# Kernel optimization log

Hardware: AMD Instinct MI355X
Metric: run time of the kernel (lower is better)

## Reference

```python
import jax, jax.numpy as jnp
import numpy as np
from jax import lax

H_LSTM = 2048

def setup_inputs() -> dict:
    key = jax.random.key(0)
    ks = jax.random.split(key, 8)
    N, T = 32, 20
    inp = {
        'base_out': jax.random.normal(ks[0], (N * T, 12, 4096), jnp.float32) * 0.1,
        'dist': jax.random.uniform(ks[1], (N, T, 2, 2, 12, 12), jnp.float32),
        'W1': jax.random.normal(ks[2], (4096, 4096), jnp.float32) * 0.02,
        'W2': jax.random.normal(ks[3], (2048, 2048), jnp.float32) * 0.02,
        'w_ih': jax.random.normal(ks[4], (4 * H_LSTM, 3072), jnp.float32) * 0.02,
        'w_hh': jax.random.normal(ks[5], (4 * H_LSTM, H_LSTM), jnp.float32) * 0.02,
        'b_ih': jnp.zeros((4 * H_LSTM,), jnp.float32),
        'b_hh': jnp.zeros((4 * H_LSTM,), jnp.float32),
        'Wc': jax.random.normal(ks[6], (8, H_LSTM), jnp.float32) * 0.01,
        'bc': jnp.zeros((8,), jnp.float32),
        'N': N,
        'T': T,
    }
    return inp

def _lstm(x, w_ih, w_hh, b_ih, b_hh):
    # x: [seq, batch, in]; torch gate order i, f, g, o
    seq, batch, _ = x.shape
    h0 = jnp.zeros((batch, H_LSTM), x.dtype)
    def step(carry, xt):
        h, c = carry
        gates = xt @ w_ih.T + b_ih + h @ w_hh.T + b_hh
        i, f, g, o = jnp.split(gates, 4, axis=-1)
        c = jax.nn.sigmoid(f) * c + jax.nn.sigmoid(i) * jnp.tanh(g)
        h = jax.nn.sigmoid(o) * jnp.tanh(c)
        return (h, c), h
    (_, _), hs = lax.scan(step, (h0, h0), x)
    return hs  # [seq, batch, H]

def reference(base_out, dist, W1, W2, w_ih, w_hh, b_ih, b_hh, Wc, bc, N, T):
    NT = N * T
    distb = dist[:, :, 1].reshape(NT, 2, 12, 12)
    distc = dist[:, :, 0].reshape(NT, 2, 12, 12)
    # conv1da: 1x1 conv == per-node linear; base_out [NT,12,4096] -> [NT,4096,12]
    node1 = jnp.einsum('oc,nvc->nov', W1, base_out).reshape(NT, 2, 2048, 12)
    n1 = jnp.einsum('nkcv,nkvw->ncw', node1, distb) + jnp.einsum('nkcv,nkvw->ncw', node1, distc)
    node1 = jax.nn.relu(n1)  # [NT,2048,12]
    node2 = jnp.einsum('oc,ncv->nov', W2, node1).reshape(NT, 2, 1024, 12)
    n2b = jax.nn.relu(jnp.einsum('nkcv,nkvw->ncw', node2, distb))  # [NT,1024,12]
    n2c = jax.nn.relu(jnp.einsum('nkcv,nkvw->ncw', node2, distc))
    left = n2b[:, :, :6].mean(axis=2)
    right = n2b[:, :, 6:].mean(axis=2)
    allf = n2c.mean(axis=2)
    pooled = jnp.concatenate([left, right, allf], axis=1).reshape(N, T, 3072)
    # torch nn.LSTM default is seq-first: sequence dim = N, batch dim = T (faithful)
    video_feat = _lstm(pooled, w_ih, w_hh, b_ih, b_hh)  # [N, T, 2048]
    group_cls = video_feat[:, -1, :] @ Wc.T + bc  # [N, num_classes]
    return group_cls, video_feat
```

## Files before the change

kernel.cpp:

```cpp
#include <hip/hip_runtime.h>

typedef _Float16 f16x8 __attribute__((ext_vector_type(8)));
typedef _Float16 f16x4 __attribute__((ext_vector_type(4)));
typedef __attribute__((ext_vector_type(4))) float f32x4;
typedef __attribute__((ext_vector_type(4))) unsigned int u32x4;

#define DI __device__ __forceinline__

DI void gload16(const void* g, void* l) {
  __builtin_amdgcn_global_load_lds(
      (const __attribute__((address_space(1))) unsigned int*)g,
      (__attribute__((address_space(3))) unsigned int*)l, 16, 0, 0);
}

DI float sigm(float x) { return 1.f / (1.f + __expf(-x)); }
DI float tanh_(float x) { return 2.f / (1.f + __expf(-2.f * x)) - 1.f; }

__global__ __launch_bounds__(256) void cvt4h(const float* __restrict__ in,
                                             _Float16* __restrict__ out, int n4) {
  int i = blockIdx.x * 256 + threadIdx.x;
  if (i >= n4) return;
  float4 v = ((const float4*)in)[i];
  f16x4 o;
  o[0] = (_Float16)v.x; o[1] = (_Float16)v.y; o[2] = (_Float16)v.z; o[3] = (_Float16)v.w;
  ((f16x4*)out)[i] = o;
}

__global__ __launch_bounds__(512, 2)
void gemm256(const _Float16* __restrict__ A, const _Float16* __restrict__ B,
             _Float16* __restrict__ C, int M, int N, int K) {
  extern __shared__ _Float16 sm[];
  _Float16* smA = sm;
  _Float16* smB = sm + 32768;

  const int t512 = threadIdx.x;
  const int lane = t512 & 63, wid = t512 >> 6;
  const int wm = (wid >> 2) * 128, wn = (wid & 3) * 64;
  const int lr = lane & 15, lg = lane >> 4;
  const int sg0 = lg ^ (lr & 7), sg1 = (4 + lg) ^ (lr & 7);

  const int nwgx = gridDim.x;
  int id = blockIdx.y * nwgx + blockIdx.x;
  int nwg = nwgx * gridDim.y;
  if ((nwg & 7) == 0) id = (id & 7) * (nwg >> 3) + (id >> 3);
  const int n0 = (id % nwgx) * 256;
  const int m0 = (id / nwgx) * 256;

  f32x4 acc[8][4] = {};

#define STAGE(kt, buf)                                                         \
  {                                                                            \
    const int kbase = (kt) * 64;                                               \
    _Pragma("unroll") for (int i = 0; i < 4; ++i) {                            \
      int G = t512 + i * 512;                                                  \
      int r = G >> 3, gs = (G & 7) ^ (r & 7);                                  \
      gload16(A + (size_t)(m0 + r) * K + kbase + gs * 8,                       \
              smA + (buf) * 16384 + G * 8);                                    \
    }                                                                          \
    _Pragma("unroll") for (int i = 0; i < 4; ++i) {                            \
      int G = t512 + i * 512;                                                  \
      int r = G >> 3, gs = (G & 7) ^ (r & 7);                                  \
      gload16(B + (size_t)(n0 + r) * K + kbase + gs * 8,                       \
              smB + (buf) * 16384 + G * 8);                                    \
    }                                                                          \
  }

#define KPHASE(SG)                                                             \
  {                                                                            \
    f16x8 av[8], bv[4];                                                        \
    _Pragma("unroll") for (int im = 0; im < 8; ++im)                           \
      av[im] = *(const f16x8*)(Ab + (wm + im * 16 + lr) * 128 + (SG) * 16);    \
    _Pragma("unroll") for (int jn = 0; jn < 4; ++jn)                           \
      bv[jn] = *(const f16x8*)(Bb + (wn + jn * 16 + lr) * 128 + (SG) * 16);    \
    __builtin_amdgcn_s_barrier();                                              \
    asm volatile("s_waitcnt lgkmcnt(0)" ::: "memory");                         \
    __builtin_amdgcn_sched_barrier(0);                                         \
    __builtin_amdgcn_s_setprio(1);                                             \
    _Pragma("unroll") for (int im = 0; im < 8; ++im)                           \
        _Pragma("unroll") for (int jn = 0; jn < 4; ++jn)                       \
      acc[im][jn] = __builtin_amdgcn_mfma_f32_16x16x32_f16(av[im], bv[jn],     \
                                                           acc[im][jn], 0, 0, 0); \
    __builtin_amdgcn_s_setprio(0);                                             \
    __builtin_amdgcn_s_barrier();                                              \
    __builtin_amdgcn_sched_barrier(0);                                         \
  }

  STAGE(0, 0);
  const int NT = K >> 6;
  for (int t = 0; t < NT; ++t) {
    const int c = t & 1;
    if (t + 1 < NT) {
      STAGE(t + 1, c ^ 1);
      asm volatile("s_waitcnt vmcnt(8)" ::: "memory");
    } else {
      asm volatile("s_waitcnt vmcnt(0)" ::: "memory");
    }
    __builtin_amdgcn_s_barrier();
    __builtin_amdgcn_sched_barrier(0);
    const char* Ab = (const char*)(smA + c * 16384);
    const char* Bb = (const char*)(smB + c * 16384);
    KPHASE(sg0)
    KPHASE(sg1)
  }
#undef STAGE
#undef KPHASE

#pragma unroll
  for (int m = 0; m < 8; ++m)
#pragma unroll
    for (int n = 0; n < 4; ++n)
#pragma unroll
      for (int q = 0; q < 4; ++q) {
        int row = m0 + wm + m * 16 + lg * 4 + q;
        int col = n0 + wn + n * 16 + lr;
        C[(size_t)row * N + col] = (_Float16)acc[m][n][q];
      }
}

template <int OUTMODE>
__global__ __launch_bounds__(256, 2)
void gemm_bt(const _Float16* __restrict__ A, const _Float16* __restrict__ B,
             void* __restrict__ Cout, const float* __restrict__ bias1,
             const float* __restrict__ bias2, int M, int N, int K) {
  __shared__ alignas(16) _Float16 Asm[128 * 32];
  __shared__ alignas(16) _Float16 Bsm[128 * 32];
  const int t = threadIdx.x;
  const int lane = t & 63, wid = t >> 6;
  const int m0 = blockIdx.y * 128, n0 = blockIdx.x * 128;
  const int wm = (wid >> 1) * 64, wn = (wid & 1) * 64;
  const int lr = lane & 15, lk = (lane >> 4) * 8, lg = lane >> 4;

  f32x4 acc[4][4] = {};

  const int e0 = t, e1 = t + 256;
  const int ra0 = e0 >> 2, ka0 = (e0 & 3) << 3;
  const int ra1 = e1 >> 2, ka1 = (e1 & 3) << 3;

  for (int kt = 0; kt < K; kt += 32) {
    gload16(A + (size_t)(m0 + ra0) * K + kt + ka0, &Asm[e0 * 8]);
    gload16(A + (size_t)(m0 + ra1) * K + kt + ka1, &Asm[e1 * 8]);
    gload16(B + (size_t)(n0 + ra0) * K + kt + ka0, &Bsm[e0 * 8]);
    gload16(B + (size_t)(n0 + ra1) * K + kt + ka1, &Bsm[e1 * 8]);
    __syncthreads();
    f16x8 af[4], bfr[4];
#pragma unroll
    for (int f = 0; f < 4; ++f) {
      af[f] = *(const f16x8*)&Asm[(wm + f * 16 + lr) * 32 + lk];
      bfr[f] = *(const f16x8*)&Bsm[(wn + f * 16 + lr) * 32 + lk];
    }
#pragma unroll
    for (int i = 0; i < 4; ++i)
#pragma unroll
      for (int j = 0; j < 4; ++j)
        acc[i][j] = __builtin_amdgcn_mfma_f32_16x16x32_f16(af[i], bfr[j], acc[i][j], 0, 0, 0);
    __syncthreads();
  }

#pragma unroll
  for (int i = 0; i < 4; ++i) {
#pragma unroll
    for (int j = 0; j < 4; ++j) {
#pragma unroll
      for (int q = 0; q < 4; ++q) {
        int row = m0 + wm + i * 16 + lg * 4 + q;
        int col = n0 + wn + j * 16 + lr;
        if constexpr (OUTMODE == 0) {
          ((_Float16*)Cout)[(size_t)row * N + col] = (_Float16)acc[i][j][q];
        } else {
          ((float*)Cout)[(size_t)row * N + col] = acc[i][j][q] + bias1[col] + bias2[col];
        }
      }
    }
  }
}

__global__ __launch_bounds__(256) void mix1(const _Float16* __restrict__ node1,
                                            const float* __restrict__ dist,
                                            _Float16* __restrict__ n1t) {
  __shared__ float ds[288];
  const int nt = blockIdx.x, tid = threadIdx.x;
  for (int i = tid; i < 288; i += 256)
    ds[i] = dist[(size_t)nt * 576 + 288 + i] + dist[(size_t)nt * 576 + i];
  __syncthreads();
  const int c = blockIdx.y * 256 + tid;
  float s[12];
#pragma unroll
  for (int w = 0; w < 12; ++w) s[w] = 0.f;
#pragma unroll
  for (int k = 0; k < 2; ++k)
#pragma unroll
    for (int v = 0; v < 12; ++v) {
      float x = (float)node1[(size_t)(nt * 12 + v) * 4096 + k * 2048 + c];
      const float* d = &ds[k * 144 + v * 12];
#pragma unroll
      for (int w = 0; w < 12; ++w) s[w] = fmaf(x, d[w], s[w]);
    }
#pragma unroll
  for (int w = 0; w < 12; ++w)
    n1t[(size_t)(nt * 12 + w) * 2048 + c] = (_Float16)fmaxf(s[w], 0.f);
}

__global__ __launch_bounds__(256) void mix2(const _Float16* __restrict__ node2,
                                            const float* __restrict__ dist,
                                            _Float16* __restrict__ pooled) {
  __shared__ float db[288], dc[288];
  const int nt = blockIdx.x, tid = threadIdx.x;
  for (int i = tid; i < 288; i += 256) {
    db[i] = dist[(size_t)nt * 576 + 288 + i];
    dc[i] = dist[(size_t)nt * 576 + i];
  }
  __syncthreads();
  const int c = blockIdx.y * 256 + tid;
  float sb[12], sc[12];
#pragma unroll
  for (int w = 0; w < 12; ++w) { sb[w] = 0.f; sc[w] = 0.f; }
#pragma unroll
  for (int k = 0; k < 2; ++k)
#pragma unroll
    for (int v = 0; v < 12; ++v) {
      float x = (float)node2[(size_t)(nt * 12 + v) * 2048 + k * 1024 + c];
      const float* pb = &db[k * 144 + v * 12];
      const float* pc = &dc[k * 144 + v * 12];
#pragma unroll
      for (int w = 0; w < 12; ++w) { sb[w] = fmaf(x, pb[w], sb[w]); sc[w] = fmaf(x, pc[w], sc[w]); }
    }
  float left = 0.f, right = 0.f, allf = 0.f;
#pragma unroll
  for (int w = 0; w < 6; ++w) left += fmaxf(sb[w], 0.f);
#pragma unroll
  for (int w = 6; w < 12; ++w) right += fmaxf(sb[w], 0.f);
#pragma unroll
  for (int w = 0; w < 12; ++w) allf += fmaxf(sc[w], 0.f);
  pooled[(size_t)nt * 3072 + c] = (_Float16)(left * (1.f / 6.f));
  pooled[(size_t)nt * 3072 + 1024 + c] = (_Float16)(right * (1.f / 6.f));
  pooled[(size_t)nt * 3072 + 2048 + c] = (_Float16)(allf * (1.f / 12.f));
}

__global__ __launch_bounds__(256, 1) void lstm_persist3(
    const _Float16* __restrict__ whh,
    const float* __restrict__ xg,
    _Float16* __restrict__ hbuf,
    float* __restrict__ vf,
    int* __restrict__ go,
    int* __restrict__ flags) {
  extern __shared__ char lds[];
  char* hls = lds;
  char* wls = lds + 81920;
  float* Y = (float*)(lds + 147456);
  const int tid = threadIdx.x, bid = blockIdx.x, cb = bid * 8;
  const int lane = tid & 63, wid = tid >> 6;
  const int mi = wid >> 1, ni = wid & 1;
  const int lr = lane & 15, lg = lane >> 4;
  const int n = ni * 16 + lr;
  const _Float16* wp = whh + (size_t)((n >> 3) * 2048 + cb + (n & 7)) * 2048;
  const int arow = mi * 16 + lr;
  const int arow_c = (arow < 20) ? arow : (16 + (lr & 3));
  const int axor = arow_c & 7;
  const int pt = tid >> 3, pj = tid & 7;
  float c_reg = 0.f;

  for (int i = tid; i < 4096; i += 256) {
    int r = i >> 8, gg = i & 255;
    u32x4 v = *(const u32x4*)(whh + (size_t)((r >> 3) * 2048 + cb + (r & 7)) * 2048 + gg * 8);
    *(u32x4*)(wls + (((r) << 8) + (gg ^ (r & 7))) * 16) = v;
  }

  for (int s = 0; s < 32; ++s) {
    if (s > 0) {
      const _Float16* hsrc = hbuf + ((s - 1) & 1) * 65536;
      u32x4 tmp[20];
#pragma unroll
      for (int j = 0; j < 20; ++j) {
        asm volatile("global_load_dwordx4 %0, %1, off sc0 sc1"
                     : "=v"(tmp[j]) : "v"(hsrc + j * 2048 + tid * 8));
      }
      asm volatile("s_waitcnt vmcnt(0)" ::: "memory");
      __builtin_amdgcn_sched_barrier(0);
#pragma unroll
      for (int j = 0; j < 20; ++j)
        *(u32x4*)(hls + (((j) << 8) + (tid ^ (j & 7))) * 16) = tmp[j];
      __syncthreads();
      f32x4 acc = {};
      if (ni == 0) {
#pragma unroll 8
        for (int kt = 0; kt < 2048; kt += 32) {
          int g = (kt >> 3) + lg;
          f16x8 a = *(const f16x8*)(hls + ((arow_c << 8) + (g ^ axor)) * 16);
          f16x8 w = *(const f16x8*)(wls + ((n << 8) + (g ^ (n & 7))) * 16);
          acc = __builtin_amdgcn_mfma_f32_16x16x32_f16(a, w, acc, 0, 0, 0);
        }
      } else {
#pragma unroll 8
        for (int kt = 0; kt < 2048; kt += 32) {
          int g = (kt >> 3) + lg;
          f16x8 a = *(const f16x8*)(hls + ((arow_c << 8) + (g ^ axor)) * 16);
          f16x8 w = *(const f16x8*)(wp + kt + lg * 8);
          acc = __builtin_amdgcn_mfma_f32_16x16x32_f16(a, w, acc, 0, 0, 0);
        }
      }
#pragma unroll
      for (int q = 0; q < 4; ++q) {
        int t = mi * 16 + lg * 4 + q;
        if (t < 20) Y[t * 32 + n] = acc[q];
      }
    }
    __syncthreads();
    if (tid < 160) {
      float g0 = xg[(size_t)(s * 20 + pt) * 8192 + cb + pj];
      float g1 = xg[(size_t)(s * 20 + pt) * 8192 + 2048 + cb + pj];
      float g2 = xg[(size_t)(s * 20 + pt) * 8192 + 4096 + cb + pj];
      float g3 = xg[(size_t)(s * 20 + pt) * 8192 + 6144 + cb + pj];
      if (s > 0) {
        g0 += Y[pt * 32 + pj];
        g1 += Y[pt * 32 + 8 + pj];
        g2 += Y[pt * 32 + 16 + pj];
        g3 += Y[pt * 32 + 24 + pj];
      }
      float cn = sigm(g1) * c_reg + sigm(g0) * tanh_(g2);
      float hv = sigm(g3) * tanh_(cn);
      c_reg = cn;
      union { _Float16 f; unsigned short u; } cv;
      cv.f = (_Float16)hv;
      int mine = cv.u;
      int oth = __shfl_xor(mine, 1, 64);
      if ((tid & 1) == 0) {
        unsigned int packed = ((unsigned)mine & 0xffffu) | ((unsigned)oth << 16);
        __hip_atomic_store((unsigned int*)(hbuf + (s & 1) * 65536 + pt * 2048 + cb + pj),
                           packed, __ATOMIC_RELAXED, __HIP_MEMORY_SCOPE_AGENT);
      }
      vf[(size_t)(s * 20 + pt) * 2048 + cb + pj] = hv;
    }
    if (s == 31) break;
    asm volatile("s_waitcnt vmcnt(0)" ::: "memory");
    __syncthreads();
    if (bid == 0) {
      if (tid > 0) {
        while (__hip_atomic_load(&flags[tid * 16], __ATOMIC_RELAXED,
                                 __HIP_MEMORY_SCOPE_AGENT) < s + 1)
          __builtin_amdgcn_s_sleep(2);
      }
      __syncthreads();
      if (tid < 8)
        __hip_atomic_store(&go[tid * 16], s + 1, __ATOMIC_RELAXED,
                           __HIP_MEMORY_SCOPE_AGENT);
    } else {
      if (tid == 0) {
        __hip_atomic_store(&flags[bid * 16], s + 1, __ATOMIC_RELAXED,
                           __HIP_MEMORY_SCOPE_AGENT);
        while (__hip_atomic_load(&go[(bid & 7) * 16], __ATOMIC_RELAXED,
                                 __HIP_MEMORY_SCOPE_AGENT) < s + 1)
          __builtin_amdgcn_s_sleep(4);
      }
      __syncthreads();
    }
  }
}

__global__ __launch_bounds__(256) void gcls(const float* __restrict__ vf,
                                            const float* __restrict__ Wc,
                                            const float* __restrict__ bc,
                                            float* __restrict__ out) {
  const int n = blockIdx.x;
  const int j = threadIdx.x >> 5, l = threadIdx.x & 31;
  const float* v = vf + (size_t)(n * 20 + 19) * 2048;
  const float* w = Wc + (size_t)j * 2048;
  float s = 0.f;
  for (int c = l; c < 2048; c += 32) s += v[c] * w[c];
  for (int off = 16; off > 0; off >>= 1) s += __shfl_down(s, off, 32);
  if (l == 0) out[n * 8 + j] = s + bc[j];
}

extern "C" void kernel_launch(void* const* d_in, const int* in_sizes, int n_in,
                              void* d_out, int out_size, void* d_ws, size_t ws_size,
                              hipStream_t stream) {
  const float* base_out = (const float*)d_in[0];
  const float* dist = (const float*)d_in[1];
  const float* W1 = (const float*)d_in[2];
  const float* W2 = (const float*)d_in[3];
  const float* w_ih = (const float*)d_in[4];
  const float* w_hh = (const float*)d_in[5];
  const float* b_ih = (const float*)d_in[6];
  const float* b_hh = (const float*)d_in[7];
  const float* Wc = (const float*)d_in[8];
  const float* bc = (const float*)d_in[9];
  float* out = (float*)d_out;

  char* ws = (char*)d_ws;
  const size_t MB = 1048576;
  _Float16* Ahf   = (_Float16*)(ws + 0);
  _Float16* W1hf  = (_Float16*)(ws + 60 * MB);
  _Float16* node1 = (_Float16*)(ws + 92 * MB);
  _Float16* whhhf = (_Float16*)(ws + 152 * MB);
  _Float16* wihhf = (_Float16*)(ws + 184 * MB);
  float* xg       = (float*)(ws + 232 * MB);
  int* go         = (int*)(ws + 252 * MB);
  int* flags      = (int*)(ws + 252 * MB + 1024);
  _Float16* hbuf  = (_Float16*)(ws + 252 * MB + 65536);
  _Float16* W2hf  = (_Float16*)(ws + 255 * MB);
  _Float16* pooled= (_Float16*)(ws + 263 * MB);
  _Float16* n1t   = (_Float16*)(ws + 0);
  _Float16* node2 = (_Float16*)(ws + 30 * MB);

  hipFuncSetAttribute((const void*)gemm256,
                      hipFuncAttributeMaxDynamicSharedMemorySize, 131072);
  hipFuncSetAttribute((const void*)lstm_persist3,
                      hipFuncAttributeMaxDynamicSharedMemorySize, 150016);

  cvt4h<<<30720, 256, 0, stream>>>(base_out, Ahf, 7864320);
  cvt4h<<<16384, 256, 0, stream>>>(W1, W1hf, 4194304);
  cvt4h<<<4096, 256, 0, stream>>>(W2, W2hf, 1048576);
  cvt4h<<<24576, 256, 0, stream>>>(w_ih, wihhf, 6291456);
  cvt4h<<<16384, 256, 0, stream>>>(w_hh, whhhf, 4194304);

  gemm256<<<dim3(16, 30), 512, 131072, stream>>>(Ahf, W1hf, node1, 7680, 4096, 4096);
  mix1<<<dim3(640, 8), 256, 0, stream>>>(node1, dist, n1t);
  gemm256<<<dim3(8, 30), 512, 131072, stream>>>(n1t, W2hf, node2, 7680, 2048, 2048);
  mix2<<<dim3(640, 4), 256, 0, stream>>>(node2, dist, pooled);
  gemm_bt<1><<<dim3(64, 5), 256, 0, stream>>>(pooled, wihhf, xg, b_ih, b_hh,
                                              640, 8192, 3072);
  hipMemsetAsync(go, 0, 65536, stream);
  lstm_persist3<<<256, 256, 150016, stream>>>(whhhf, xg, hbuf, out + 256, go, flags);
  gcls<<<32, 256, 0, stream>>>(out + 256, Wc, bc, out);
}
```

Before: 834.8 us.

## Restructure GEMM main loop into four sub-tile phases with interleaved prefetch

Reorganizes the 256x256 fp16 GEMM inner loop into four quadrant phases (8 MFMAs per k-slice pair each). LDS fragment loads for the next quadrant and global-to-LDS prefetch of the next K tile (A then B) are spread across the phases. This cuts register use for fragments and aims to overlap memory traffic with MFMA work. It adds more barriers per iteration and requires a full vmcnt(0) wait at the end of every iteration.

```diff
diff --git a/kernel.cpp b/kernel.cpp
--- a/kernel.cpp
+++ b/kernel.cpp
@@ -48,7 +48,7 @@
 
   f32x4 acc[8][4] = {};
 
-#define STAGE(kt, buf)                                                         \
+#define STAGE_A(kt, buf)                                                       \
   {                                                                            \
     const int kbase = (kt) * 64;                                               \
     _Pragma("unroll") for (int i = 0; i < 4; ++i) {                            \
@@ -57,6 +57,10 @@
       gload16(A + (size_t)(m0 + r) * K + kbase + gs * 8,                       \
               smA + (buf) * 16384 + G * 8);                                    \
     }                                                                          \
+  }
+#define STAGE_B(kt, buf)                                                       \
+  {                                                                            \
+    const int kbase = (kt) * 64;                                               \
     _Pragma("unroll") for (int i = 0; i < 4; ++i) {                            \
       int G = t512 + i * 512;                                                  \
       int r = G >> 3, gs = (G & 7) ^ (r & 7);                                  \
@@ -65,45 +69,87 @@
     }                                                                          \
   }
 
-#define KPHASE(SG)                                                             \
-  {                                                                            \
-    f16x8 av[8], bv[4];                                                        \
-    _Pragma("unroll") for (int im = 0; im < 8; ++im)                           \
-      av[im] = *(const f16x8*)(Ab + (wm + im * 16 + lr) * 128 + (SG) * 16);    \
-    _Pragma("unroll") for (int jn = 0; jn < 4; ++jn)                           \
-      bv[jn] = *(const f16x8*)(Bb + (wn + jn * 16 + lr) * 128 + (SG) * 16);    \
-    __builtin_amdgcn_s_barrier();                                              \
-    asm volatile("s_waitcnt lgkmcnt(0)" ::: "memory");                         \
-    __builtin_amdgcn_sched_barrier(0);                                         \
-    __builtin_amdgcn_s_setprio(1);                                             \
-    _Pragma("unroll") for (int im = 0; im < 8; ++im)                           \
-        _Pragma("unroll") for (int jn = 0; jn < 4; ++jn)                       \
-      acc[im][jn] = __builtin_amdgcn_mfma_f32_16x16x32_f16(av[im], bv[jn],     \
-                                                           acc[im][jn], 0, 0, 0); \
-    __builtin_amdgcn_s_setprio(0);                                             \
-    __builtin_amdgcn_s_barrier();                                              \
-    __builtin_amdgcn_sched_barrier(0);                                         \
-  }
-
-  STAGE(0, 0);
+#define MFMA_Q(IMB, JNB)                                                       \
+  __builtin_amdgcn_s_setprio(1);                                               \
+  _Pragma("unroll") for (int im = 0; im < 4; ++im)                             \
+      _Pragma("unroll") for (int jn = 0; jn < 2; ++jn) {                       \
+    acc[(IMB) + im][(JNB) + jn] = __builtin_amdgcn_mfma_f32_16x16x32_f16(      \
+        av[im][0], bv[jn][0], acc[(IMB) + im][(JNB) + jn], 0, 0, 0);           \
+    acc[(IMB) + im][(JNB) + jn] = __builtin_amdgcn_mfma_f32_16x16x32_f16(      \
+        av[im][1], bv[jn][1], acc[(IMB) + im][(JNB) + jn], 0, 0, 0);           \
+  }                                                                            \
+  __builtin_amdgcn_s_setprio(0);
+
+#define BAR_IN  __builtin_amdgcn_s_barrier();                                  \
+                asm volatile("s_waitcnt lgkmcnt(0)" ::: "memory");             \
+                __builtin_amdgcn_sched_barrier(0);
+#define BAR_OUT __builtin_amdgcn_s_barrier();                                  \
+                __builtin_amdgcn_sched_barrier(0);
+
+  STAGE_A(0, 0)
+  STAGE_B(0, 0)
+  asm volatile("s_waitcnt vmcnt(0)" ::: "memory");
+  __builtin_amdgcn_s_barrier();
+  __builtin_amdgcn_sched_barrier(0);
+
   const int NT = K >> 6;
   for (int t = 0; t < NT; ++t) {
     const int c = t & 1;
-    if (t + 1 < NT) {
-      STAGE(t + 1, c ^ 1);
-      asm volatile("s_waitcnt vmcnt(8)" ::: "memory");
-    } else {
-      asm volatile("s_waitcnt vmcnt(0)" ::: "memory");
-    }
-    __builtin_amdgcn_s_barrier();
-    __builtin_amdgcn_sched_barrier(0);
     const char* Ab = (const char*)(smA + c * 16384);
     const char* Bb = (const char*)(smB + c * 16384);
-    KPHASE(sg0)
-    KPHASE(sg1)
-  }
-#undef STAGE
-#undef KPHASE
+    const bool pre = (t + 1 < NT);
+    f16x8 av[4][2], bv[2][2];
+#pragma unroll
+    for (int im = 0; im < 4; ++im) {
+      int row = wm + im * 16 + lr;
+      av[im][0] = *(const f16x8*)(Ab + row * 128 + sg0 * 16);
+      av[im][1] = *(const f16x8*)(Ab + row * 128 + sg1 * 16);
+    }
+#pragma unroll
+    for (int jn = 0; jn < 2; ++jn) {
+      int row = wn + jn * 16 + lr;
+      bv[jn][0] = *(const f16x8*)(Bb + row * 128 + sg0 * 16);
+      bv[jn][1] = *(const f16x8*)(Bb + row * 128 + sg1 * 16);
+    }
+    if (pre) STAGE_A(t + 1, c ^ 1)
+    BAR_IN
+    MFMA_Q(0, 0)
+    BAR_OUT
+#pragma unroll
+    for (int jn = 0; jn < 2; ++jn) {
+      int row = wn + (2 + jn) * 16 + lr;
+      bv[jn][0] = *(const f16x8*)(Bb + row * 128 + sg0 * 16);
+      bv[jn][1] = *(const f16x8*)(Bb + row * 128 + sg1 * 16);
+    }
+    if (pre) STAGE_B(t + 1, c ^ 1)
+    BAR_IN
+    MFMA_Q(0, 2)
+    BAR_OUT
+#pragma unroll
+    for (int im = 0; im < 4; ++im) {
+      int row = wm + (4 + im) * 16 + lr;
+      av[im][0] = *(const f16x8*)(Ab + row * 128 + sg0 * 16);
+      av[im][1] = *(const f16x8*)(Ab + row * 128 + sg1 * 16);
+    }
+    BAR_IN
+    MFMA_Q(4, 2)
+    BAR_OUT
+#pragma unroll
+    for (int jn = 0; jn < 2; ++jn) {
+      int row = wn + jn * 16 + lr;
+      bv[jn][0] = *(const f16x8*)(Bb + row * 128 + sg0 * 16);
+      bv[jn][1] = *(const f16x8*)(Bb + row * 128 + sg1 * 16);
+    }
+    BAR_IN
+    MFMA_Q(4, 0)
+    asm volatile("s_waitcnt vmcnt(0)" ::: "memory");
+    BAR_OUT
+  }
+#undef STAGE_A
+#undef STAGE_B
+#undef MFMA_Q
+#undef BAR_IN
+#undef BAR_OUT
 
 #pragma unroll
   for (int m = 0; m < 8; ++m)
```

New measurement: 798.5 us. -4.3%, faster.

## Restructure gemm256 main loop into quadrant-interleaved load/MFMA pipeline

Applied to the files above, without the earlier changes.

Replaces the two-phase-per-tile loop in the 256x256 GEMM with an 8-stage schedule per pair of K tiles. Each stage reads a quarter of the A/B fragments, issues a slice of the next tile's global-to-LDS loads, and runs 16 MFMAs, so global loads are spread across the compute instead of issued in one burst. The goal is finer overlap of memory and MFMA work, in the style of ping-pong schedules. The cost is more barriers, tighter vmcnt bookkeeping, and the risk of LDS hazards, since slices of a buffer are refilled while other parts of it are still being read.

```diff
diff --git a/kernel.cpp b/kernel.cpp
--- a/kernel.cpp
+++ b/kernel.cpp
@@ -38,6 +38,7 @@
   const int wm = (wid >> 2) * 128, wn = (wid & 3) * 64;
   const int lr = lane & 15, lg = lane >> 4;
   const int sg0 = lg ^ (lr & 7), sg1 = (4 + lg) ^ (lr & 7);
+  const int so = lane >> 3, sgr = lane & 7;
 
   const int nwgx = gridDim.x;
   int id = blockIdx.y * nwgx + blockIdx.x;
@@ -48,62 +49,110 @@
 
   f32x4 acc[8][4] = {};
 
-#define STAGE(kt, buf)                                                         \
-  {                                                                            \
-    const int kbase = (kt) * 64;                                               \
-    _Pragma("unroll") for (int i = 0; i < 4; ++i) {                            \
-      int G = t512 + i * 512;                                                  \
-      int r = G >> 3, gs = (G & 7) ^ (r & 7);                                  \
-      gload16(A + (size_t)(m0 + r) * K + kbase + gs * 8,                       \
-              smA + (buf) * 16384 + G * 8);                                    \
-    }                                                                          \
-    _Pragma("unroll") for (int i = 0; i < 4; ++i) {                            \
-      int G = t512 + i * 512;                                                  \
-      int r = G >> 3, gs = (G & 7) ^ (r & 7);                                  \
-      gload16(B + (size_t)(n0 + r) * K + kbase + gs * 8,                       \
-              smB + (buf) * 16384 + G * 8);                                    \
-    }                                                                          \
-  }
-
-#define KPHASE(SG)                                                             \
-  {                                                                            \
-    f16x8 av[8], bv[4];                                                        \
-    _Pragma("unroll") for (int im = 0; im < 8; ++im)                           \
-      av[im] = *(const f16x8*)(Ab + (wm + im * 16 + lr) * 128 + (SG) * 16);    \
-    _Pragma("unroll") for (int jn = 0; jn < 4; ++jn)                           \
-      bv[jn] = *(const f16x8*)(Bb + (wn + jn * 16 + lr) * 128 + (SG) * 16);    \
-    __builtin_amdgcn_s_barrier();                                              \
-    asm volatile("s_waitcnt lgkmcnt(0)" ::: "memory");                         \
-    __builtin_amdgcn_sched_barrier(0);                                         \
-    __builtin_amdgcn_s_setprio(1);                                             \
-    _Pragma("unroll") for (int im = 0; im < 8; ++im)                           \
-        _Pragma("unroll") for (int jn = 0; jn < 4; ++jn)                       \
-      acc[im][jn] = __builtin_amdgcn_mfma_f32_16x16x32_f16(av[im], bv[jn],     \
-                                                           acc[im][jn], 0, 0, 0); \
-    __builtin_amdgcn_s_setprio(0);                                             \
-    __builtin_amdgcn_s_barrier();                                              \
-    __builtin_amdgcn_sched_barrier(0);                                         \
-  }
-
-  STAGE(0, 0);
-  const int NT = K >> 6;
-  for (int t = 0; t < NT; ++t) {
-    const int c = t & 1;
-    if (t + 1 < NT) {
-      STAGE(t + 1, c ^ 1);
-      asm volatile("s_waitcnt vmcnt(8)" ::: "memory");
+#define STG_A(u, kt, b)                                                        \
+  { _Pragma("unroll") for (int i_ = 0; i_ < 2; ++i_) {                         \
+      int s_ = i_ * 8 + wid;                                                   \
+      int o_ = ((s_ >> 3) << 4) + (u) * 8 + (s_ & 7);                          \
+      int pr_ = o_ * 8 + so;                                                   \
+      gload16(A + (size_t)(m0 + pr_) * K + (kt) * 64 + (sgr ^ (pr_ & 7)) * 8,  \
+              smA + (b) * 16384 + o_ * 512 + lane * 8); } }
+#define STG_B(u, kt, b)                                                        \
+  { _Pragma("unroll") for (int i_ = 0; i_ < 2; ++i_) {                         \
+      int s_ = i_ * 8 + wid;                                                   \
+      int o_ = ((s_ >> 2) << 3) + (u) * 4 + (s_ & 3);                          \
+      int pr_ = o_ * 8 + so;                                                   \
+      gload16(B + (size_t)(n0 + pr_) * K + (kt) * 64 + (sgr ^ (pr_ & 7)) * 8,  \
+              smB + (b) * 16384 + o_ * 512 + lane * 8); } }
+
+#define RD_A03(Xb) _Pragma("unroll") for (int f_ = 0; f_ < 4; ++f_) {          \
+    int row = wm + f_ * 16 + lr;                                               \
+    av0[f_][0] = *(const f16x8*)((Xb) + row * 128 + sg0 * 16);                 \
+    av0[f_][1] = *(const f16x8*)((Xb) + row * 128 + sg1 * 16); }
+#define RD_A47(Xb) _Pragma("unroll") for (int f_ = 0; f_ < 4; ++f_) {          \
+    int row = wm + (4 + f_) * 16 + lr;                                         \
+    av1[f_][0] = *(const f16x8*)((Xb) + row * 128 + sg0 * 16);                 \
+    av1[f_][1] = *(const f16x8*)((Xb) + row * 128 + sg1 * 16); }
+#define RD_B01(Xb) _Pragma("unroll") for (int j_ = 0; j_ < 2; ++j_) {          \
+    int row = wn + j_ * 16 + lr;                                               \
+    bv0[j_][0] = *(const f16x8*)((Xb) + row * 128 + sg0 * 16);                 \
+    bv0[j_][1] = *(const f16x8*)((Xb) + row * 128 + sg1 * 16); }
+#define RD_B23(Xb) _Pragma("unroll") for (int j_ = 0; j_ < 2; ++j_) {          \
+    int row = wn + (2 + j_) * 16 + lr;                                         \
+    bv1[j_][0] = *(const f16x8*)((Xb) + row * 128 + sg0 * 16);                 \
+    bv1[j_][1] = *(const f16x8*)((Xb) + row * 128 + sg1 * 16); }
+
+#define MQ(AV, BV, FB, NB)                                                     \
+  __builtin_amdgcn_s_setprio(1);                                               \
+  _Pragma("unroll") for (int f_ = 0; f_ < 4; ++f_)                             \
+  _Pragma("unroll") for (int j_ = 0; j_ < 2; ++j_) {                           \
+    acc[(FB) + f_][(NB) + j_] = __builtin_amdgcn_mfma_f32_16x16x32_f16(        \
+        AV[f_][0], BV[j_][0], acc[(FB) + f_][(NB) + j_], 0, 0, 0);             \
+    acc[(FB) + f_][(NB) + j_] = __builtin_amdgcn_mfma_f32_16x16x32_f16(        \
+        AV[f_][1], BV[j_][1], acc[(FB) + f_][(NB) + j_], 0, 0, 0); }           \
+  __builtin_amdgcn_s_setprio(0);
+
+#define BARIN  __builtin_amdgcn_s_barrier();                                   \
+               asm volatile("s_waitcnt lgkmcnt(0)" ::: "memory");              \
+               __builtin_amdgcn_sched_barrier(0);
+#define BAROUT __builtin_amdgcn_s_barrier();                                   \
+               __builtin_amdgcn_sched_barrier(0);
+
+  const char* Ab0 = (const char*)smA;
+  const char* Ab1 = (const char*)(smA + 16384);
+  const char* Bb0 = (const char*)smB;
+  const char* Bb1 = (const char*)(smB + 16384);
+
+  STG_A(0, 0, 0) STG_B(0, 0, 0) STG_B(1, 0, 0) STG_A(1, 0, 0)
+  STG_A(0, 1, 1) STG_B(0, 1, 1) STG_B(1, 1, 1)
+  asm volatile("s_waitcnt vmcnt(6)" ::: "memory");
+  __builtin_amdgcn_s_barrier();
+  __builtin_amdgcn_sched_barrier(0);
+
+  const int NI = K >> 7;
+  f16x8 av0[4][2], av1[4][2], bv0[2][2], bv1[2][2];
+  for (int it = 0; it < NI; ++it) {
+    const int tb = 2 * it + 1, sa = 2 * it + 2, sb = 2 * it + 3;
+    const bool pre = (it + 1 < NI);
+    RD_A03(Ab0) RD_B01(Bb0)
+    STG_A(1, tb, 1)
+    BARIN  MQ(av0, bv0, 0, 0)  BAROUT
+    RD_B23(Bb0)
+    if (pre) STG_A(0, sa, 0)
+    BARIN  MQ(av0, bv1, 0, 2)  BAROUT
+    RD_A47(Ab0)
+    if (pre) STG_B(0, sa, 0)
+    BARIN  MQ(av1, bv1, 4, 2)  BAROUT
+    if (pre) {
+      STG_B(1, sa, 0)
+      asm volatile("s_waitcnt vmcnt(6)" ::: "memory");
     } else {
       asm volatile("s_waitcnt vmcnt(0)" ::: "memory");
     }
-    __builtin_amdgcn_s_barrier();
-    __builtin_amdgcn_sched_barrier(0);
-    const char* Ab = (const char*)(smA + c * 16384);
-    const char* Bb = (const char*)(smB + c * 16384);
-    KPHASE(sg0)
-    KPHASE(sg1)
-  }
-#undef STAGE
-#undef KPHASE
+    BARIN  MQ(av1, bv0, 4, 0)  BAROUT
+    RD_A03(Ab1) RD_B01(Bb1)
+    if (pre) STG_A(1, sa, 0)
+    BARIN  MQ(av0, bv0, 0, 0)  BAROUT
+    RD_B23(Bb1)
+    if (pre) STG_A(0, sb, 1)
+    BARIN  MQ(av0, bv1, 0, 2)  BAROUT
+    RD_A47(Ab1)
+    if (pre) STG_B(0, sb, 1)
+    BARIN  MQ(av1, bv1, 4, 2)  BAROUT
+    if (pre) {
+      STG_B(1, sb, 1)
+      asm volatile("s_waitcnt vmcnt(6)" ::: "memory");
+    }
+    BARIN  MQ(av1, bv0, 4, 0)  BAROUT
+  }
+#undef STG_A
+#undef STG_B
+#undef RD_A03
+#undef RD_A47
+#undef RD_B01
+#undef RD_B23
+#undef MQ
+#undef BARIN
+#undef BAROUT
 
 #pragma unroll
   for (int m = 0; m < 8; ++m)
```

Result: faster. 783.0 us (-6.2%).
